# Performance work log

Measured on AMD Instinct MI355X. Metric: run time of the kernel, lower is better.

The kernel has to match this reference:

```python
import jax, jax.numpy as jnp
import numpy as np

NUM_STEPS = 32
INIT_TH = 0.125      # encoder initial threshold (args.threshold)
ENC_GROW = 2.0       # burst coding threshold growth factor
LIF_BETA = 0.9       # args.beta
LIF_TH = 1.0         # snn.Leaky default threshold
HIDDEN = 50
NUM_CLASSES = 5
DATA_STEPS = 187


def spike_fn(x):
    # Heaviside spike (forward only)
    return (x > 0).astype(x.dtype)


def setup_inputs() -> dict:
    key = jax.random.key(0)
    k1, k2, k3 = jax.random.split(key, 3)
    B = 16384
    x = jax.random.uniform(k1, (B, DATA_STEPS), dtype=jnp.float32)
    W1 = jax.random.normal(k2, (HIDDEN, DATA_STEPS), dtype=jnp.float32) * (1.0 / np.sqrt(DATA_STEPS))
    W2 = jax.random.normal(k3, (NUM_CLASSES, HIDDEN), dtype=jnp.float32) * (1.0 / np.sqrt(HIDDEN))
    return {"x": x, "W1": W1, "W2": W2}


def reference(x, W1, W2):
    B = x.shape[0]
    dt = x.dtype

    def step(carry, _):
        r, th, mem1, mem2 = carry
        # BURST encoder: spike when residual crosses adaptive threshold
        spk_in = (r >= th).astype(dt)                 # [B, D]
        r = r - spk_in * th
        th = jnp.where(spk_in > 0, th * ENC_GROW, jnp.asarray(INIT_TH, dt))
        # layer 1: linear + Leaky LIF (reset by subtraction)
        cur1 = spk_in @ W1.T                          # [B, 50]
        mem1 = LIF_BETA * mem1 + cur1
        spk1 = spike_fn(mem1 - LIF_TH)
        mem1 = mem1 - spk1 * LIF_TH
        # layer 2
        cur2 = spk1 @ W2.T                            # [B, C]
        mem2 = LIF_BETA * mem2 + cur2
        spk2 = spike_fn(mem2 - LIF_TH)
        mem2 = mem2 - spk2 * LIF_TH
        return (r, th, mem1, mem2), (spk2, spk_in.sum(1))

    carry0 = (
        x,
        jnp.full_like(x, INIT_TH),
        jnp.zeros((B, HIDDEN), dt),
        jnp.zeros((B, NUM_CLASSES), dt),
    )
    _, (spk_rec, counts) = jax.lax.scan(step, carry0, None, length=NUM_STEPS)
    # spk_rec: [T, B, C]; spike_count: [B]
    return spk_rec, counts.sum(0)
```

## Files before the change

kernel.cpp:

```cpp
#include <hip/hip_runtime.h>


constexpr int D = 187;
constexpr int H = 50;
constexpr int C = 5;
constexpr int T = 32;
constexpr int WPB = 16;
constexpr int ROWS1 = 193;
constexpr int RS = 64;

__device__ __forceinline__ int v_ffbl(unsigned int m) {
    int r;
    asm("v_ffbl_b32 %0, %1" : "=v"(r) : "v"(m));
    return r;
}

__device__ __forceinline__ void pk_add(float2& acc, float2 w) {
    asm("v_pk_add_f32 %0, %1, %0" : "+v"(acc) : "v"(w));
}

__device__ __forceinline__ void pk_fma(float2& m, float2 a, float2 c) {
    asm("v_pk_fma_f32 %0, %1, %0, %2" : "+v"(m) : "v"(a), "v"(c));
}

__device__ __forceinline__ void pk_fma_b(float2& acc, float2 s, float2 w) {
    asm("v_pk_fma_f32 %0, %2, %1, %0 op_sel:[0,0,0] op_sel_hi:[0,1,1]"
        : "+v"(acc) : "v"(w), "v"(s));
}

__device__ __forceinline__ float2 sw16(float2 v) {
    float2 r;
    r.x = __int_as_float(__builtin_amdgcn_ds_swizzle(__float_as_int(v.x), 0x401F));
    r.y = __int_as_float(__builtin_amdgcn_ds_swizzle(__float_as_int(v.y), 0x401F));
    return r;
}

__global__ __launch_bounds__(1024, 8)
void burst_snn_kernel(const float* __restrict__ x,
                      const float* __restrict__ W1,
                      const float* __restrict__ W2,
                      float* __restrict__ out, int B) {
    __shared__ float Wt1[ROWS1 * RS];
    __shared__ float Wt2[1024];

    const int tid = threadIdx.x;
    for (int idx = tid; idx < ROWS1 * RS; idx += 1024) {
        int rd = idx >> 6, j = idx & 63;
        int g = rd / 33;
        bool zrow = (rd == 33 * g);
        int d = rd - 1 - g;
        int slot = j >> 2, c = j & 3;
        int h = 13 * c + slot;
        float v = 0.f;
        if (!zrow && slot < 13 && h < H) v = W1[h * D + d];
        Wt1[idx] = v;
    }
    {
        int r = tid >> 4, c = tid & 15;
        int h = -1;
        if (r >= 1 && r <= 25) h = r - 1;
        else if (r >= 27 && r <= 51) h = r - 2;
        float v = 0.f;
        if (h >= 0 && c < C) v = W2[c * H + h];
        Wt2[tid] = v;
    }
    __syncthreads();

    const int lane = tid & 63;
    const int b = blockIdx.x * WPB + (tid >> 6);
    const bool active = b < B;
    const bool isLo = lane < 32;
    const int qOdd = (lane >> 4) & 1;
    const int ql = lane & 15;

    const char* wb = (const char*)Wt1;
    const int qbase = ql * 16 + (qOdd ? (33 << 8) : 0) + 256;
    const char* bs0 = wb + qbase;
    const char* bs1 = wb + qbase + (66 << 8);
    const char* bs2 = wb + qbase + (132 << 8);

    const float* base2 = Wt2 + ((qOdd ? 27 : 1) << 4) + ql;

    float r0 = 0.f, r1 = 0.f, r2 = 0.f;
    if (active) {
        const float* xb = x + (size_t)b * D;
        r0 = xb[lane];
        r1 = xb[64 + lane];
        if (lane < D - 128) r2 = xb[128 + lane];
    }
    float th0 = 0.125f, th1 = 0.125f, th2 = 0.125f;
    float2 m01 = make_float2(0.f, 0.f), m23 = make_float2(0.f, 0.f);
    float mem2 = 0.f;
    int cnt = 0;

    const float2 beta2 = make_float2(0.9f, 0.9f);
    const float2 neg1 = make_float2(-1.0f, -1.0f);

    float* outSpk = out;
    float* outCnt = out + (size_t)T * B * C;
    const unsigned BC = (unsigned)(B * C);
    unsigned o0 = (unsigned)(b * C + lane);

    unsigned int ga[6], gb[6];
    int tDone = T;

    for (int t = 0; t < T; t += 2) {
        {
            bool s0 = r0 >= th0, s1 = r1 >= th1, s2 = r2 >= th2;
            r0 -= s0 ? th0 : 0.f; th0 = s0 ? th0 + th0 : 0.125f;
            r1 -= s1 ? th1 : 0.f; th1 = s1 ? th1 + th1 : 0.125f;
            r2 -= s2 ? th2 : 0.f; th2 = s2 ? th2 + th2 : 0.125f;
            unsigned long long B0 = __ballot(s0), B1 = __ballot(s1), B2 = __ballot(s2);
            ga[0] = (unsigned)B0; ga[1] = (unsigned)(B0 >> 32);
            ga[2] = (unsigned)B1; ga[3] = (unsigned)(B1 >> 32);
            ga[4] = (unsigned)B2; ga[5] = (unsigned)(B2 >> 32);
        }
        {
            bool s0 = r0 >= th0, s1 = r1 >= th1, s2 = r2 >= th2;
            r0 -= s0 ? th0 : 0.f; th0 = s0 ? th0 + th0 : 0.125f;
            r1 -= s1 ? th1 : 0.f; th1 = s1 ? th1 + th1 : 0.125f;
            r2 -= s2 ? th2 : 0.f; th2 = s2 ? th2 + th2 : 0.125f;
            unsigned long long B0 = __ballot(s0), B1 = __ballot(s1), B2 = __ballot(s2);
            gb[0] = (unsigned)B0; gb[1] = (unsigned)(B0 >> 32);
            gb[2] = (unsigned)B1; gb[3] = (unsigned)(B1 >> 32);
            gb[4] = (unsigned)B2; gb[5] = (unsigned)(B2 >> 32);
        }

        int pa0 = __popc(ga[0]), pa1 = __popc(ga[1]), pa2 = __popc(ga[2]);
        int pa3 = __popc(ga[3]), pa4 = __popc(ga[4]), pa5 = __popc(ga[5]);
        int pb0 = __popc(gb[0]), pb1 = __popc(gb[1]), pb2 = __popc(gb[2]);
        int pb3 = __popc(gb[3]), pb4 = __popc(gb[4]), pb5 = __popc(gb[5]);
        cnt += pa0 + pa1 + pa2 + pa3 + pa4 + pa5
             + pb0 + pb1 + pb2 + pb3 + pb4 + pb5;
        int n = pa0 > pa1 ? pa0 : pa1;
        n = n > pa2 ? n : pa2;  n = n > pa3 ? n : pa3;
        n = n > pa4 ? n : pa4;  n = n > pa5 ? n : pa5;
        n = n > pb0 ? n : pb0;  n = n > pb1 ? n : pb1;
        n = n > pb2 ? n : pb2;  n = n > pb3 ? n : pb3;
        n = n > pb4 ? n : pb4;  n = n > pb5 ? n : pb5;

        unsigned e0 = isLo ? ga[0] : gb[0], d0 = isLo ? ga[1] : gb[1];
        unsigned e1 = isLo ? ga[2] : gb[2], d1 = isLo ? ga[3] : gb[3];
        unsigned e2 = isLo ? ga[4] : gb[4], d2 = isLo ? ga[5] : gb[5];
        unsigned vm0 = qOdd ? d0 : e0;
        unsigned vm1 = qOdd ? d1 : e1;
        unsigned vm2 = qOdd ? d2 : e2;

        float2 a0l = {0.f, 0.f}, a0h = {0.f, 0.f};
        float2 a1l = {0.f, 0.f}, a1h = {0.f, 0.f};
        float2 a2l = {0.f, 0.f}, a2h = {0.f, 0.f};
        if (n >= 21) {
            float2 sv0 = {0.f, 0.f}, sv1 = {0.f, 0.f}, sv2 = {0.f, 0.f};
            #pragma unroll
            for (int f = 0; f < 32; ++f) {
                sv0.x = (float)((vm0 >> f) & 1u);
                sv1.x = (float)((vm1 >> f) & 1u);
                sv2.x = (float)((vm2 >> f) & 1u);
                const char* p0 = bs0 + (f << 8);
                const char* p1 = bs1 + (f << 8);
                const char* p2 = bs2 + (f << 8);
                float2 w0l = *(const float2*)p0, w0h = *(const float2*)(p0 + 8);
                float2 w1l = *(const float2*)p1, w1h = *(const float2*)(p1 + 8);
                float2 w2l = *(const float2*)p2, w2h = *(const float2*)(p2 + 8);
                pk_fma_b(a0l, sv0, w0l); pk_fma_b(a0h, sv0, w0h);
                pk_fma_b(a1l, sv1, w1l); pk_fma_b(a1h, sv1, w1h);
                pk_fma_b(a2l, sv2, w2l); pk_fma_b(a2h, sv2, w2h);
            }
        } else {
            for (; n > 0; --n) {
                int f0 = v_ffbl(vm0); vm0 &= vm0 - 1;
                int f1 = v_ffbl(vm1); vm1 &= vm1 - 1;
                int f2 = v_ffbl(vm2); vm2 &= vm2 - 1;
                const char* p0 = bs0 + (f0 << 8);
                const char* p1 = bs1 + (f1 << 8);
                const char* p2 = bs2 + (f2 << 8);
                float2 w0l = *(const float2*)p0, w0h = *(const float2*)(p0 + 8);
                float2 w1l = *(const float2*)p1, w1h = *(const float2*)(p1 + 8);
                float2 w2l = *(const float2*)p2, w2h = *(const float2*)(p2 + 8);
                pk_add(a0l, w0l); pk_add(a0h, w0h);
                pk_add(a1l, w1l); pk_add(a1h, w1h);
                pk_add(a2l, w2l); pk_add(a2h, w2h);
            }
        }

        float2 s0l = sw16(a0l), s0h = sw16(a0h);
        float2 s1l = sw16(a1l), s1h = sw16(a1h);
        float2 s2l = sw16(a2l), s2h = sw16(a2h);
        float2 cml = a0l, cmh = a0h;
        pk_add(cml, s0l); pk_add(cmh, s0h);
        pk_add(cml, a1l); pk_add(cmh, a1h);
        pk_add(cml, s1l); pk_add(cmh, s1h);
        pk_add(cml, a2l); pk_add(cmh, a2h);
        pk_add(cml, s2l); pk_add(cmh, s2h);
        float2 cu01 = make_float2(__shfl_down(cml.x, 32), __shfl_down(cml.y, 32));
        float2 cu23 = make_float2(__shfl_down(cmh.x, 32), __shfl_down(cmh.y, 32));

        pk_fma(m01, beta2, cml);
        pk_fma(m23, beta2, cmh);
        float2 d01 = m01, d23 = m23;
        pk_add(d01, neg1); pk_add(d23, neg1);
        bool t0 = d01.x > 0.f, t1 = d01.y > 0.f;
        bool t2 = d23.x > 0.f, t3 = d23.y > 0.f;
        unsigned long long Pa = __ballot(t0), Pb = __ballot(t1);
        unsigned long long Pc = __ballot(t2), Pd = __ballot(t3);
        m01.x = t0 ? d01.x : m01.x;  m01.y = t1 ? d01.y : m01.y;
        m23.x = t2 ? d23.x : m23.x;  m23.y = t3 ? d23.y : m23.y;
        unsigned c0t = (unsigned)Pa & 0x1FFFu;
        unsigned c1t = (unsigned)Pb & 0x1FFFu;
        unsigned c2t = (unsigned)Pc & 0x1FFFu;
        unsigned c3t = (unsigned)Pd & 0x1FFFu;
        pk_fma(m01, beta2, cu01);
        pk_fma(m23, beta2, cu23);
        float2 e01 = m01, e23 = m23;
        pk_add(e01, neg1); pk_add(e23, neg1);
        bool u0 = e01.x > 0.f, u1 = e01.y > 0.f;
        bool u2 = e23.x > 0.f, u3 = e23.y > 0.f;
        unsigned long long Qa = __ballot(u0), Qb = __ballot(u1);
        unsigned long long Qc = __ballot(u2), Qd = __ballot(u3);
        m01.x = u0 ? e01.x : m01.x;  m01.y = u1 ? e01.y : m01.y;
        m23.x = u2 ? e23.x : m23.x;  m23.y = u3 ? e23.y : m23.y;
        unsigned c0u = (unsigned)Qa & 0x1FFFu;
        unsigned c1u = (unsigned)Qb & 0x1FFFu;
        unsigned c2u = (unsigned)Qc & 0x1FFFu;
        unsigned c3u = (unsigned)Qd & 0x1FFFu;

        unsigned lo_t = c0t | ((c1t & 0xFFFu) << 13);
        unsigned hi_t = (c1t >> 12) | (c2t << 1) | ((c3t & 0x7FFu) << 14);
        unsigned lo_u = c0u | ((c1u & 0xFFFu) << 13);
        unsigned hi_u = (c1u >> 12) | (c2u << 1) | ((c3u & 0x7FFu) << 14);

        int p0c = __popc(lo_t), p1c = __popc(hi_t);
        int p2c = __popc(lo_u), p3c = __popc(hi_u);
        int n2 = p0c > p1c ? p0c : p1c;
        n2 = n2 > p2c ? n2 : p2c;
        n2 = n2 > p3c ? n2 : p3c;
        float cq = 0.f;
        if (n2) {
            unsigned vmq = isLo ? (qOdd ? hi_t : lo_t) : (qOdd ? hi_u : lo_u);
            for (; n2 > 0; --n2) {
                int f = v_ffbl(vmq); vmq &= vmq - 1;
                cq += *(base2 + f * 16);
            }
        }
        float tmp = cq + __shfl_down(cq, 16);
        float cur2 = tmp;
        float c2t1 = __shfl_down(tmp, 32);

        mem2 = 0.9f * mem2 + cur2;
        bool sp2 = (mem2 - 1.0f > 0.f);
        mem2 -= sp2 ? 1.0f : 0.f;
        if (active && lane < C) outSpk[o0] = sp2 ? 1.0f : 0.0f;
        mem2 = 0.9f * mem2 + c2t1;
        bool sp2b = (mem2 - 1.0f > 0.f);
        mem2 -= sp2b ? 1.0f : 0.f;
        if (active && lane < C) outSpk[o0 + BC] = sp2b ? 1.0f : 0.0f;
        o0 += 2u * BC;

        unsigned encAny = ga[0] | ga[1] | ga[2] | ga[3] | ga[4] | ga[5]
                        | gb[0] | gb[1] | gb[2] | gb[3] | gb[4] | gb[5];
        unsigned l1Any = lo_t | hi_t | lo_u | hi_u;
        if ((encAny | l1Any) == 0u) {
            float rm = fmaxf(fmaxf(r0, r1), r2);
            unsigned long long am = __ballot(rm >= 0.125f);
            float mm = fmaxf(fmaxf(m01.x, m01.y), fmaxf(m23.x, m23.y));
            unsigned long long m1 = __ballot(mm > 1.0f) & 0x1FFFull;
            unsigned long long m2 = __ballot(mem2 > 1.0f) & 0x1Full;
            if ((am | m1 | m2) == 0ull) { tDone = t + 2; break; }
        }
    }

    if (active && lane < C) {
        for (int tt = tDone; tt < T; ++tt) {
            outSpk[o0] = 0.0f;
            o0 += BC;
        }
    }
    if (active && lane == 0) outCnt[b] = (float)cnt;
}

extern "C" void kernel_launch(void* const* d_in, const int* in_sizes, int n_in,
                              void* d_out, int out_size, void* d_ws, size_t ws_size,
                              hipStream_t stream) {
    const float* x  = (const float*)d_in[0];
    const float* W1 = (const float*)d_in[1];
    const float* W2 = (const float*)d_in[2];
    float* out = (float*)d_out;
    const int B = in_sizes[0] / D;
    const int blocks = (B + WPB - 1) / WPB;
    burst_snn_kernel<<<blocks, 1024, 0, stream>>>(x, W1, W2, out, B);
}
```

Before: 121.3 us.

## Process two batch rows per wavefront, each half-wave owning one row

Each 64-lane wave now handles two samples instead of one: the lower and upper 32 lanes each hold one row's 187 inputs across six registers. Layer-1 work pairs the two samples within one time step instead of pairing two time steps of one sample, and the output write, spike count and early-exit masks are split per half-wave. This halves the number of blocks and is meant to spread the serial time-step and sparse-gather overhead over twice as many samples. In exchange each lane carries more registers, and the data-dependent gather loop count becomes the max over two samples, so it may run longer.

Measured after the change: 122.7 us. No clear change (+1.1%).

```diff
diff --git a/kernel.cpp b/kernel.cpp
--- a/kernel.cpp
+++ b/kernel.cpp
@@ -6,6 +6,7 @@
 constexpr int C = 5;
 constexpr int T = 32;
 constexpr int WPB = 16;
+constexpr int EPB = WPB * 2;
 constexpr int ROWS1 = 193;
 constexpr int RS = 64;
 
@@ -67,9 +68,10 @@
     __syncthreads();
 
     const int lane = tid & 63;
-    const int b = blockIdx.x * WPB + (tid >> 6);
+    const int laneH = lane & 31;
+    const bool isLo = lane < 32;
+    const int b = blockIdx.x * EPB + ((tid >> 6) << 1) + (isLo ? 0 : 1);
     const bool active = b < B;
-    const bool isLo = lane < 32;
     const int qOdd = (lane >> 4) & 1;
     const int ql = lane & 15;
 
@@ -81,17 +83,21 @@
 
     const float* base2 = Wt2 + ((qOdd ? 27 : 1) << 4) + ql;
 
-    float r0 = 0.f, r1 = 0.f, r2 = 0.f;
+    float r0 = 0.f, r1 = 0.f, r2 = 0.f, r3 = 0.f, r4 = 0.f, r5 = 0.f;
     if (active) {
         const float* xb = x + (size_t)b * D;
-        r0 = xb[lane];
-        r1 = xb[64 + lane];
-        if (lane < D - 128) r2 = xb[128 + lane];
+        r0 = xb[laneH];
+        r1 = xb[32 + laneH];
+        r2 = xb[64 + laneH];
+        r3 = xb[96 + laneH];
+        r4 = xb[128 + laneH];
+        if (laneH < D - 160) r5 = xb[160 + laneH];
     }
     float th0 = 0.125f, th1 = 0.125f, th2 = 0.125f;
+    float th3 = 0.125f, th4 = 0.125f, th5 = 0.125f;
     float2 m01 = make_float2(0.f, 0.f), m23 = make_float2(0.f, 0.f);
     float mem2 = 0.f;
-    int cnt = 0;
+    int cntA = 0, cntB = 0;
 
     const float2 beta2 = make_float2(0.9f, 0.9f);
     const float2 neg1 = make_float2(-1.0f, -1.0f);
@@ -99,53 +105,12 @@
     float* outSpk = out;
     float* outCnt = out + (size_t)T * B * C;
     const unsigned BC = (unsigned)(B * C);
-    unsigned o0 = (unsigned)(b * C + lane);
-
-    unsigned int ga[6], gb[6];
+    unsigned o0 = (unsigned)(b * C + laneH);
+
     int tDone = T;
 
-    for (int t = 0; t < T; t += 2) {
-        {
-            bool s0 = r0 >= th0, s1 = r1 >= th1, s2 = r2 >= th2;
-            r0 -= s0 ? th0 : 0.f; th0 = s0 ? th0 + th0 : 0.125f;
-            r1 -= s1 ? th1 : 0.f; th1 = s1 ? th1 + th1 : 0.125f;
-            r2 -= s2 ? th2 : 0.f; th2 = s2 ? th2 + th2 : 0.125f;
-            unsigned long long B0 = __ballot(s0), B1 = __ballot(s1), B2 = __ballot(s2);
-            ga[0] = (unsigned)B0; ga[1] = (unsigned)(B0 >> 32);
-            ga[2] = (unsigned)B1; ga[3] = (unsigned)(B1 >> 32);
-            ga[4] = (unsigned)B2; ga[5] = (unsigned)(B2 >> 32);
-        }
-        {
-            bool s0 = r0 >= th0, s1 = r1 >= th1, s2 = r2 >= th2;
-            r0 -= s0 ? th0 : 0.f; th0 = s0 ? th0 + th0 : 0.125f;
-            r1 -= s1 ? th1 : 0.f; th1 = s1 ? th1 + th1 : 0.125f;
-            r2 -= s2 ? th2 : 0.f; th2 = s2 ? th2 + th2 : 0.125f;
-            unsigned long long B0 = __ballot(s0), B1 = __ballot(s1), B2 = __ballot(s2);
-            gb[0] = (unsigned)B0; gb[1] = (unsigned)(B0 >> 32);
-            gb[2] = (unsigned)B1; gb[3] = (unsigned)(B1 >> 32);
-            gb[4] = (unsigned)B2; gb[5] = (unsigned)(B2 >> 32);
-        }
-
-        int pa0 = __popc(ga[0]), pa1 = __popc(ga[1]), pa2 = __popc(ga[2]);
-        int pa3 = __popc(ga[3]), pa4 = __popc(ga[4]), pa5 = __popc(ga[5]);
-        int pb0 = __popc(gb[0]), pb1 = __popc(gb[1]), pb2 = __popc(gb[2]);
-        int pb3 = __popc(gb[3]), pb4 = __popc(gb[4]), pb5 = __popc(gb[5]);
-        cnt += pa0 + pa1 + pa2 + pa3 + pa4 + pa5
-             + pb0 + pb1 + pb2 + pb3 + pb4 + pb5;
-        int n = pa0 > pa1 ? pa0 : pa1;
-        n = n > pa2 ? n : pa2;  n = n > pa3 ? n : pa3;
-        n = n > pa4 ? n : pa4;  n = n > pa5 ? n : pa5;
-        n = n > pb0 ? n : pb0;  n = n > pb1 ? n : pb1;
-        n = n > pb2 ? n : pb2;  n = n > pb3 ? n : pb3;
-        n = n > pb4 ? n : pb4;  n = n > pb5 ? n : pb5;
-
-        unsigned e0 = isLo ? ga[0] : gb[0], d0 = isLo ? ga[1] : gb[1];
-        unsigned e1 = isLo ? ga[2] : gb[2], d1 = isLo ? ga[3] : gb[3];
-        unsigned e2 = isLo ? ga[4] : gb[4], d2 = isLo ? ga[5] : gb[5];
-        unsigned vm0 = qOdd ? d0 : e0;
-        unsigned vm1 = qOdd ? d1 : e1;
-        unsigned vm2 = qOdd ? d2 : e2;
-
+    auto gather = [&](unsigned vm0, unsigned vm1, unsigned vm2, int n,
+                      float2& cml, float2& cmh) {
         float2 a0l = {0.f, 0.f}, a0h = {0.f, 0.f};
         float2 a1l = {0.f, 0.f}, a1h = {0.f, 0.f};
         float2 a2l = {0.f, 0.f}, a2h = {0.f, 0.f};
@@ -182,19 +147,19 @@
                 pk_add(a2l, w2l); pk_add(a2h, w2h);
             }
         }
-
         float2 s0l = sw16(a0l), s0h = sw16(a0h);
         float2 s1l = sw16(a1l), s1h = sw16(a1h);
         float2 s2l = sw16(a2l), s2h = sw16(a2h);
-        float2 cml = a0l, cmh = a0h;
+        cml = a0l; cmh = a0h;
         pk_add(cml, s0l); pk_add(cmh, s0h);
         pk_add(cml, a1l); pk_add(cmh, a1h);
         pk_add(cml, s1l); pk_add(cmh, s1h);
         pk_add(cml, a2l); pk_add(cmh, a2h);
         pk_add(cml, s2l); pk_add(cmh, s2h);
-        float2 cu01 = make_float2(__shfl_down(cml.x, 32), __shfl_down(cml.y, 32));
-        float2 cu23 = make_float2(__shfl_down(cmh.x, 32), __shfl_down(cmh.y, 32));
-
+    };
+
+    auto lif1 = [&](float2 cml, float2 cmh, unsigned& loA, unsigned& hiA,
+                    unsigned& loB, unsigned& hiB) {
         pk_fma(m01, beta2, cml);
         pk_fma(m23, beta2, cmh);
         float2 d01 = m01, d23 = m23;
@@ -205,77 +170,151 @@
         unsigned long long Pc = __ballot(t2), Pd = __ballot(t3);
         m01.x = t0 ? d01.x : m01.x;  m01.y = t1 ? d01.y : m01.y;
         m23.x = t2 ? d23.x : m23.x;  m23.y = t3 ? d23.y : m23.y;
-        unsigned c0t = (unsigned)Pa & 0x1FFFu;
-        unsigned c1t = (unsigned)Pb & 0x1FFFu;
-        unsigned c2t = (unsigned)Pc & 0x1FFFu;
-        unsigned c3t = (unsigned)Pd & 0x1FFFu;
-        pk_fma(m01, beta2, cu01);
-        pk_fma(m23, beta2, cu23);
-        float2 e01 = m01, e23 = m23;
-        pk_add(e01, neg1); pk_add(e23, neg1);
-        bool u0 = e01.x > 0.f, u1 = e01.y > 0.f;
-        bool u2 = e23.x > 0.f, u3 = e23.y > 0.f;
-        unsigned long long Qa = __ballot(u0), Qb = __ballot(u1);
-        unsigned long long Qc = __ballot(u2), Qd = __ballot(u3);
-        m01.x = u0 ? e01.x : m01.x;  m01.y = u1 ? e01.y : m01.y;
-        m23.x = u2 ? e23.x : m23.x;  m23.y = u3 ? e23.y : m23.y;
-        unsigned c0u = (unsigned)Qa & 0x1FFFu;
-        unsigned c1u = (unsigned)Qb & 0x1FFFu;
-        unsigned c2u = (unsigned)Qc & 0x1FFFu;
-        unsigned c3u = (unsigned)Qd & 0x1FFFu;
-
-        unsigned lo_t = c0t | ((c1t & 0xFFFu) << 13);
-        unsigned hi_t = (c1t >> 12) | (c2t << 1) | ((c3t & 0x7FFu) << 14);
-        unsigned lo_u = c0u | ((c1u & 0xFFFu) << 13);
-        unsigned hi_u = (c1u >> 12) | (c2u << 1) | ((c3u & 0x7FFu) << 14);
-
-        int p0c = __popc(lo_t), p1c = __popc(hi_t);
-        int p2c = __popc(lo_u), p3c = __popc(hi_u);
-        int n2 = p0c > p1c ? p0c : p1c;
-        n2 = n2 > p2c ? n2 : p2c;
-        n2 = n2 > p3c ? n2 : p3c;
+        unsigned cA0 = (unsigned)Pa & 0x1FFFu, cB0 = (unsigned)(Pa >> 32) & 0x1FFFu;
+        unsigned cA1 = (unsigned)Pb & 0x1FFFu, cB1 = (unsigned)(Pb >> 32) & 0x1FFFu;
+        unsigned cA2 = (unsigned)Pc & 0x1FFFu, cB2 = (unsigned)(Pc >> 32) & 0x1FFFu;
+        unsigned cA3 = (unsigned)Pd & 0x1FFFu, cB3 = (unsigned)(Pd >> 32) & 0x1FFFu;
+        loA = cA0 | ((cA1 & 0xFFFu) << 13);
+        hiA = (cA1 >> 12) | (cA2 << 1) | ((cA3 & 0x7FFu) << 14);
+        loB = cB0 | ((cB1 & 0xFFFu) << 13);
+        hiB = (cB1 >> 12) | (cB2 << 1) | ((cB3 & 0x7FFu) << 14);
+    };
+
+    auto l2step = [&](unsigned loA, unsigned hiA, unsigned loB, unsigned hiB) {
+        int p0 = __popc(loA), p1 = __popc(hiA);
+        int p2 = __popc(loB), p3 = __popc(hiB);
+        int n2 = p0 > p1 ? p0 : p1;
+        n2 = n2 > p2 ? n2 : p2;
+        n2 = n2 > p3 ? n2 : p3;
         float cq = 0.f;
         if (n2) {
-            unsigned vmq = isLo ? (qOdd ? hi_t : lo_t) : (qOdd ? hi_u : lo_u);
+            unsigned vmq = isLo ? (qOdd ? hiA : loA) : (qOdd ? hiB : loB);
             for (; n2 > 0; --n2) {
                 int f = v_ffbl(vmq); vmq &= vmq - 1;
                 cq += *(base2 + f * 16);
             }
         }
-        float tmp = cq + __shfl_down(cq, 16);
-        float cur2 = tmp;
-        float c2t1 = __shfl_down(tmp, 32);
-
+        float cur2 = cq + __shfl_down(cq, 16);
         mem2 = 0.9f * mem2 + cur2;
         bool sp2 = (mem2 - 1.0f > 0.f);
         mem2 -= sp2 ? 1.0f : 0.f;
-        if (active && lane < C) outSpk[o0] = sp2 ? 1.0f : 0.0f;
-        mem2 = 0.9f * mem2 + c2t1;
-        bool sp2b = (mem2 - 1.0f > 0.f);
-        mem2 -= sp2b ? 1.0f : 0.f;
-        if (active && lane < C) outSpk[o0 + BC] = sp2b ? 1.0f : 0.0f;
-        o0 += 2u * BC;
-
-        unsigned encAny = ga[0] | ga[1] | ga[2] | ga[3] | ga[4] | ga[5]
-                        | gb[0] | gb[1] | gb[2] | gb[3] | gb[4] | gb[5];
-        unsigned l1Any = lo_t | hi_t | lo_u | hi_u;
-        if ((encAny | l1Any) == 0u) {
-            float rm = fmaxf(fmaxf(r0, r1), r2);
+        if (active && laneH < C) outSpk[o0] = sp2 ? 1.0f : 0.0f;
+        o0 += BC;
+    };
+
+    for (int t = 0; t < T; t += 2) {
+        unsigned long long E0, E1, E2, E3, E4, E5;
+        {
+            bool s0 = r0 >= th0, s1 = r1 >= th1, s2 = r2 >= th2;
+            bool s3 = r3 >= th3, s4 = r4 >= th4, s5 = r5 >= th5;
+            r0 -= s0 ? th0 : 0.f; th0 = s0 ? th0 + th0 : 0.125f;
+            r1 -= s1 ? th1 : 0.f; th1 = s1 ? th1 + th1 : 0.125f;
+            r2 -= s2 ? th2 : 0.f; th2 = s2 ? th2 + th2 : 0.125f;
+            r3 -= s3 ? th3 : 0.f; th3 = s3 ? th3 + th3 : 0.125f;
+            r4 -= s4 ? th4 : 0.f; th4 = s4 ? th4 + th4 : 0.125f;
+            r5 -= s5 ? th5 : 0.f; th5 = s5 ? th5 + th5 : 0.125f;
+            E0 = __ballot(s0); E1 = __ballot(s1); E2 = __ballot(s2);
+            E3 = __ballot(s3); E4 = __ballot(s4); E5 = __ballot(s5);
+        }
+        unsigned long long F0, F1, F2, F3, F4, F5;
+        {
+            bool s0 = r0 >= th0, s1 = r1 >= th1, s2 = r2 >= th2;
+            bool s3 = r3 >= th3, s4 = r4 >= th4, s5 = r5 >= th5;
+            r0 -= s0 ? th0 : 0.f; th0 = s0 ? th0 + th0 : 0.125f;
+            r1 -= s1 ? th1 : 0.f; th1 = s1 ? th1 + th1 : 0.125f;
+            r2 -= s2 ? th2 : 0.f; th2 = s2 ? th2 + th2 : 0.125f;
+            r3 -= s3 ? th3 : 0.f; th3 = s3 ? th3 + th3 : 0.125f;
+            r4 -= s4 ? th4 : 0.f; th4 = s4 ? th4 + th4 : 0.125f;
+            r5 -= s5 ? th5 : 0.f; th5 = s5 ? th5 + th5 : 0.125f;
+            F0 = __ballot(s0); F1 = __ballot(s1); F2 = __ballot(s2);
+            F3 = __ballot(s3); F4 = __ballot(s4); F5 = __ballot(s5);
+        }
+
+        unsigned At0 = (unsigned)E0, Bt0 = (unsigned)(E0 >> 32);
+        unsigned At1 = (unsigned)E1, Bt1 = (unsigned)(E1 >> 32);
+        unsigned At2 = (unsigned)E2, Bt2 = (unsigned)(E2 >> 32);
+        unsigned At3 = (unsigned)E3, Bt3 = (unsigned)(E3 >> 32);
+        unsigned At4 = (unsigned)E4, Bt4 = (unsigned)(E4 >> 32);
+        unsigned At5 = (unsigned)E5, Bt5 = (unsigned)(E5 >> 32);
+        unsigned Au0 = (unsigned)F0, Bu0 = (unsigned)(F0 >> 32);
+        unsigned Au1 = (unsigned)F1, Bu1 = (unsigned)(F1 >> 32);
+        unsigned Au2 = (unsigned)F2, Bu2 = (unsigned)(F2 >> 32);
+        unsigned Au3 = (unsigned)F3, Bu3 = (unsigned)(F3 >> 32);
+        unsigned Au4 = (unsigned)F4, Bu4 = (unsigned)(F4 >> 32);
+        unsigned Au5 = (unsigned)F5, Bu5 = (unsigned)(F5 >> 32);
+
+        int qa0 = __popc(At0), qa1 = __popc(At1), qa2 = __popc(At2);
+        int qa3 = __popc(At3), qa4 = __popc(At4), qa5 = __popc(At5);
+        int qb0 = __popc(Bt0), qb1 = __popc(Bt1), qb2 = __popc(Bt2);
+        int qb3 = __popc(Bt3), qb4 = __popc(Bt4), qb5 = __popc(Bt5);
+        int ra0 = __popc(Au0), ra1 = __popc(Au1), ra2 = __popc(Au2);
+        int ra3 = __popc(Au3), ra4 = __popc(Au4), ra5 = __popc(Au5);
+        int rb0 = __popc(Bu0), rb1 = __popc(Bu1), rb2 = __popc(Bu2);
+        int rb3 = __popc(Bu3), rb4 = __popc(Bu4), rb5 = __popc(Bu5);
+        cntA += qa0 + qa1 + qa2 + qa3 + qa4 + qa5
+              + ra0 + ra1 + ra2 + ra3 + ra4 + ra5;
+        cntB += qb0 + qb1 + qb2 + qb3 + qb4 + qb5
+              + rb0 + rb1 + rb2 + rb3 + rb4 + rb5;
+        int nt = qa0 > qa1 ? qa0 : qa1;
+        nt = nt > qa2 ? nt : qa2;  nt = nt > qa3 ? nt : qa3;
+        nt = nt > qa4 ? nt : qa4;  nt = nt > qa5 ? nt : qa5;
+        nt = nt > qb0 ? nt : qb0;  nt = nt > qb1 ? nt : qb1;
+        nt = nt > qb2 ? nt : qb2;  nt = nt > qb3 ? nt : qb3;
+        nt = nt > qb4 ? nt : qb4;  nt = nt > qb5 ? nt : qb5;
+        int nu = ra0 > ra1 ? ra0 : ra1;
+        nu = nu > ra2 ? nu : ra2;  nu = nu > ra3 ? nu : ra3;
+        nu = nu > ra4 ? nu : ra4;  nu = nu > ra5 ? nu : ra5;
+        nu = nu > rb0 ? nu : rb0;  nu = nu > rb1 ? nu : rb1;
+        nu = nu > rb2 ? nu : rb2;  nu = nu > rb3 ? nu : rb3;
+        nu = nu > rb4 ? nu : rb4;  nu = nu > rb5 ? nu : rb5;
+
+        unsigned g0 = isLo ? At0 : Bt0, g1 = isLo ? At1 : Bt1;
+        unsigned g2 = isLo ? At2 : Bt2, g3 = isLo ? At3 : Bt3;
+        unsigned g4 = isLo ? At4 : Bt4, g5 = isLo ? At5 : Bt5;
+        unsigned vmt0 = qOdd ? g1 : g0;
+        unsigned vmt1 = qOdd ? g3 : g2;
+        unsigned vmt2 = qOdd ? g5 : g4;
+
+        float2 cml, cmh;
+        gather(vmt0, vmt1, vmt2, nt, cml, cmh);
+        unsigned loAt, hiAt, loBt, hiBt;
+        lif1(cml, cmh, loAt, hiAt, loBt, hiBt);
+
+        unsigned h0 = isLo ? Au0 : Bu0, h1 = isLo ? Au1 : Bu1;
+        unsigned h2 = isLo ? Au2 : Bu2, h3 = isLo ? Au3 : Bu3;
+        unsigned h4 = isLo ? Au4 : Bu4, h5 = isLo ? Au5 : Bu5;
+        unsigned vmu0 = qOdd ? h1 : h0;
+        unsigned vmu1 = qOdd ? h3 : h2;
+        unsigned vmu2 = qOdd ? h5 : h4;
+
+        gather(vmu0, vmu1, vmu2, nu, cml, cmh);
+        unsigned loAu, hiAu, loBu, hiBu;
+        lif1(cml, cmh, loAu, hiAu, loBu, hiBu);
+
+        l2step(loAt, hiAt, loBt, hiBt);
+        l2step(loAu, hiAu, loBu, hiBu);
+
+        unsigned long long encAny = E0 | E1 | E2 | E3 | E4 | E5
+                                  | F0 | F1 | F2 | F3 | F4 | F5;
+        unsigned l1Any = loAt | hiAt | loBt | hiBt
+                       | loAu | hiAu | loBu | hiBu;
+        if ((encAny | (unsigned long long)l1Any) == 0ull) {
+            float rm = fmaxf(fmaxf(fmaxf(r0, r1), fmaxf(r2, r3)), fmaxf(r4, r5));
             unsigned long long am = __ballot(rm >= 0.125f);
             float mm = fmaxf(fmaxf(m01.x, m01.y), fmaxf(m23.x, m23.y));
-            unsigned long long m1 = __ballot(mm > 1.0f) & 0x1FFFull;
-            unsigned long long m2 = __ballot(mem2 > 1.0f) & 0x1Full;
+            unsigned long long m1 = __ballot(mm > 1.0f) & 0x00001FFF00001FFFull;
+            unsigned long long m2 = __ballot(mem2 > 1.0f) & 0x0000001F0000001Full;
             if ((am | m1 | m2) == 0ull) { tDone = t + 2; break; }
         }
     }
 
-    if (active && lane < C) {
+    if (active && laneH < C) {
         for (int tt = tDone; tt < T; ++tt) {
             outSpk[o0] = 0.0f;
             o0 += BC;
         }
     }
-    if (active && lane == 0) outCnt[b] = (float)cnt;
+    if (active && laneH == 0) outCnt[b] = (float)(isLo ? cntA : cntB);
 }
 
 extern "C" void kernel_launch(void* const* d_in, const int* in_sizes, int n_in,
@@ -286,6 +325,6 @@
     const float* W2 = (const float*)d_in[2];
     float* out = (float*)d_out;
     const int B = in_sizes[0] / D;
-    const int blocks = (B + WPB - 1) / WPB;
+    const int blocks = (B + EPB - 1) / EPB;
     burst_snn_kernel<<<blocks, 1024, 0, stream>>>(x, W1, W2, out, B);
 }
```

## Use persistent blocks with atomic work-stealing over batch rows

Applied to the files above, without the earlier changes.

Switches from one wavefront per row with a full grid to a persistent grid capped at 512 blocks. Each wavefront claims its next batch row through a global atomic counter, which is reset with a memset in the workspace before launch. The aim is to balance work across rows whose early-exit times differ and to build the LDS weight tables once per block instead of once per 16 rows. It adds an atomic per row, an extra memset launch, and a loop-carried register state that could lower occupancy.

New measurement: 267.5 us. +120.5%, slower.

```diff
diff --git a/kernel.cpp b/kernel.cpp
--- a/kernel.cpp
+++ b/kernel.cpp
@@ -39,7 +39,8 @@
 void burst_snn_kernel(const float* __restrict__ x,
                       const float* __restrict__ W1,
                       const float* __restrict__ W2,
-                      float* __restrict__ out, int B) {
+                      float* __restrict__ out,
+                      int* __restrict__ counter, int B) {
     __shared__ float Wt1[ROWS1 * RS];
     __shared__ float Wt2[1024];
 
@@ -67,8 +68,6 @@
     __syncthreads();
 
     const int lane = tid & 63;
-    const int b = blockIdx.x * WPB + (tid >> 6);
-    const bool active = b < B;
     const bool isLo = lane < 32;
     const int qOdd = (lane >> 4) & 1;
     const int ql = lane & 15;
@@ -81,201 +80,207 @@
 
     const float* base2 = Wt2 + ((qOdd ? 27 : 1) << 4) + ql;
 
-    float r0 = 0.f, r1 = 0.f, r2 = 0.f;
-    if (active) {
-        const float* xb = x + (size_t)b * D;
-        r0 = xb[lane];
-        r1 = xb[64 + lane];
-        if (lane < D - 128) r2 = xb[128 + lane];
-    }
-    float th0 = 0.125f, th1 = 0.125f, th2 = 0.125f;
-    float2 m01 = make_float2(0.f, 0.f), m23 = make_float2(0.f, 0.f);
-    float mem2 = 0.f;
-    int cnt = 0;
-
     const float2 beta2 = make_float2(0.9f, 0.9f);
     const float2 neg1 = make_float2(-1.0f, -1.0f);
 
     float* outSpk = out;
     float* outCnt = out + (size_t)T * B * C;
     const unsigned BC = (unsigned)(B * C);
-    unsigned o0 = (unsigned)(b * C + lane);
-
-    unsigned int ga[6], gb[6];
-    int tDone = T;
-
-    for (int t = 0; t < T; t += 2) {
-        {
-            bool s0 = r0 >= th0, s1 = r1 >= th1, s2 = r2 >= th2;
-            r0 -= s0 ? th0 : 0.f; th0 = s0 ? th0 + th0 : 0.125f;
-            r1 -= s1 ? th1 : 0.f; th1 = s1 ? th1 + th1 : 0.125f;
-            r2 -= s2 ? th2 : 0.f; th2 = s2 ? th2 + th2 : 0.125f;
-            unsigned long long B0 = __ballot(s0), B1 = __ballot(s1), B2 = __ballot(s2);
-            ga[0] = (unsigned)B0; ga[1] = (unsigned)(B0 >> 32);
-            ga[2] = (unsigned)B1; ga[3] = (unsigned)(B1 >> 32);
-            ga[4] = (unsigned)B2; ga[5] = (unsigned)(B2 >> 32);
+    const int Bstart = gridDim.x * WPB;
+
+    int b = blockIdx.x * WPB + (tid >> 6);
+
+    while (b < B) {
+        const float* xb = x + (size_t)b * D;
+        float r0 = xb[lane];
+        float r1 = xb[64 + lane];
+        float r2 = (lane < D - 128) ? xb[128 + lane] : 0.f;
+        float th0 = 0.125f, th1 = 0.125f, th2 = 0.125f;
+        float2 m01 = make_float2(0.f, 0.f), m23 = make_float2(0.f, 0.f);
+        float mem2 = 0.f;
+        int cnt = 0;
+        unsigned o0 = (unsigned)(b * C + lane);
+        unsigned int ga[6], gb[6];
+        int tDone = T;
+
+        for (int t = 0; t < T; t += 2) {
+            {
+                bool s0 = r0 >= th0, s1 = r1 >= th1, s2 = r2 >= th2;
+                r0 -= s0 ? th0 : 0.f; th0 = s0 ? th0 + th0 : 0.125f;
+                r1 -= s1 ? th1 : 0.f; th1 = s1 ? th1 + th1 : 0.125f;
+                r2 -= s2 ? th2 : 0.f; th2 = s2 ? th2 + th2 : 0.125f;
+                unsigned long long B0 = __ballot(s0), B1 = __ballot(s1), B2 = __ballot(s2);
+                ga[0] = (unsigned)B0; ga[1] = (unsigned)(B0 >> 32);
+                ga[2] = (unsigned)B1; ga[3] = (unsigned)(B1 >> 32);
+                ga[4] = (unsigned)B2; ga[5] = (unsigned)(B2 >> 32);
+            }
+            {
+                bool s0 = r0 >= th0, s1 = r1 >= th1, s2 = r2 >= th2;
+                r0 -= s0 ? th0 : 0.f; th0 = s0 ? th0 + th0 : 0.125f;
+                r1 -= s1 ? th1 : 0.f; th1 = s1 ? th1 + th1 : 0.125f;
+                r2 -= s2 ? th2 : 0.f; th2 = s2 ? th2 + th2 : 0.125f;
+                unsigned long long B0 = __ballot(s0), B1 = __ballot(s1), B2 = __ballot(s2);
+                gb[0] = (unsigned)B0; gb[1] = (unsigned)(B0 >> 32);
+                gb[2] = (unsigned)B1; gb[3] = (unsigned)(B1 >> 32);
+                gb[4] = (unsigned)B2; gb[5] = (unsigned)(B2 >> 32);
+            }
+
+            int pa0 = __popc(ga[0]), pa1 = __popc(ga[1]), pa2 = __popc(ga[2]);
+            int pa3 = __popc(ga[3]), pa4 = __popc(ga[4]), pa5 = __popc(ga[5]);
+            int pb0 = __popc(gb[0]), pb1 = __popc(gb[1]), pb2 = __popc(gb[2]);
+            int pb3 = __popc(gb[3]), pb4 = __popc(gb[4]), pb5 = __popc(gb[5]);
+            cnt += pa0 + pa1 + pa2 + pa3 + pa4 + pa5
+                 + pb0 + pb1 + pb2 + pb3 + pb4 + pb5;
+            int n = pa0 > pa1 ? pa0 : pa1;
+            n = n > pa2 ? n : pa2;  n = n > pa3 ? n : pa3;
+            n = n > pa4 ? n : pa4;  n = n > pa5 ? n : pa5;
+            n = n > pb0 ? n : pb0;  n = n > pb1 ? n : pb1;
+            n = n > pb2 ? n : pb2;  n = n > pb3 ? n : pb3;
+            n = n > pb4 ? n : pb4;  n = n > pb5 ? n : pb5;
+
+            unsigned e0 = isLo ? ga[0] : gb[0], d0 = isLo ? ga[1] : gb[1];
+            unsigned e1 = isLo ? ga[2] : gb[2], d1 = isLo ? ga[3] : gb[3];
+            unsigned e2 = isLo ? ga[4] : gb[4], d2 = isLo ? ga[5] : gb[5];
+            unsigned vm0 = qOdd ? d0 : e0;
+            unsigned vm1 = qOdd ? d1 : e1;
+            unsigned vm2 = qOdd ? d2 : e2;
+
+            float2 a0l = {0.f, 0.f}, a0h = {0.f, 0.f};
+            float2 a1l = {0.f, 0.f}, a1h = {0.f, 0.f};
+            float2 a2l = {0.f, 0.f}, a2h = {0.f, 0.f};
+            if (n >= 21) {
+                float2 sv0 = {0.f, 0.f}, sv1 = {0.f, 0.f}, sv2 = {0.f, 0.f};
+                #pragma unroll
+                for (int f = 0; f < 32; ++f) {
+                    sv0.x = (float)((vm0 >> f) & 1u);
+                    sv1.x = (float)((vm1 >> f) & 1u);
+                    sv2.x = (float)((vm2 >> f) & 1u);
+                    const char* p0 = bs0 + (f << 8);
+                    const char* p1 = bs1 + (f << 8);
+                    const char* p2 = bs2 + (f << 8);
+                    float2 w0l = *(const float2*)p0, w0h = *(const float2*)(p0 + 8);
+                    float2 w1l = *(const float2*)p1, w1h = *(const float2*)(p1 + 8);
+                    float2 w2l = *(const float2*)p2, w2h = *(const float2*)(p2 + 8);
+                    pk_fma_b(a0l, sv0, w0l); pk_fma_b(a0h, sv0, w0h);
+                    pk_fma_b(a1l, sv1, w1l); pk_fma_b(a1h, sv1, w1h);
+                    pk_fma_b(a2l, sv2, w2l); pk_fma_b(a2h, sv2, w2h);
+                }
+            } else {
+                for (; n > 0; --n) {
+                    int f0 = v_ffbl(vm0); vm0 &= vm0 - 1;
+                    int f1 = v_ffbl(vm1); vm1 &= vm1 - 1;
+                    int f2 = v_ffbl(vm2); vm2 &= vm2 - 1;
+                    const char* p0 = bs0 + (f0 << 8);
+                    const char* p1 = bs1 + (f1 << 8);
+                    const char* p2 = bs2 + (f2 << 8);
+                    float2 w0l = *(const float2*)p0, w0h = *(const float2*)(p0 + 8);
+                    float2 w1l = *(const float2*)p1, w1h = *(const float2*)(p1 + 8);
+                    float2 w2l = *(const float2*)p2, w2h = *(const float2*)(p2 + 8);
+                    pk_add(a0l, w0l); pk_add(a0h, w0h);
+                    pk_add(a1l, w1l); pk_add(a1h, w1h);
+                    pk_add(a2l, w2l); pk_add(a2h, w2h);
+                }
+            }
+
+            float2 s0l = sw16(a0l), s0h = sw16(a0h);
+            float2 s1l = sw16(a1l), s1h = sw16(a1h);
+            float2 s2l = sw16(a2l), s2h = sw16(a2h);
+            float2 cml = a0l, cmh = a0h;
+            pk_add(cml, s0l); pk_add(cmh, s0h);
+            pk_add(cml, a1l); pk_add(cmh, a1h);
+            pk_add(cml, s1l); pk_add(cmh, s1h);
+            pk_add(cml, a2l); pk_add(cmh, a2h);
+            pk_add(cml, s2l); pk_add(cmh, s2h);
+            float2 cu01 = make_float2(__shfl_down(cml.x, 32), __shfl_down(cml.y, 32));
+            float2 cu23 = make_float2(__shfl_down(cmh.x, 32), __shfl_down(cmh.y, 32));
+
+            pk_fma(m01, beta2, cml);
+            pk_fma(m23, beta2, cmh);
+            float2 d01 = m01, d23 = m23;
+            pk_add(d01, neg1); pk_add(d23, neg1);
+            bool t0 = d01.x > 0.f, t1 = d01.y > 0.f;
+            bool t2 = d23.x > 0.f, t3 = d23.y > 0.f;
+            unsigned long long Pa = __ballot(t0), Pb = __ballot(t1);
+            unsigned long long Pc = __ballot(t2), Pd = __ballot(t3);
+            m01.x = t0 ? d01.x : m01.x;  m01.y = t1 ? d01.y : m01.y;
+            m23.x = t2 ? d23.x : m23.x;  m23.y = t3 ? d23.y : m23.y;
+            unsigned c0t = (unsigned)Pa & 0x1FFFu;
+            unsigned c1t = (unsigned)Pb & 0x1FFFu;
+            unsigned c2t = (unsigned)Pc & 0x1FFFu;
+            unsigned c3t = (unsigned)Pd & 0x1FFFu;
+            pk_fma(m01, beta2, cu01);
+            pk_fma(m23, beta2, cu23);
+            float2 e01 = m01, e23 = m23;
+            pk_add(e01, neg1); pk_add(e23, neg1);
+            bool u0 = e01.x > 0.f, u1 = e01.y > 0.f;
+            bool u2 = e23.x > 0.f, u3 = e23.y > 0.f;
+            unsigned long long Qa = __ballot(u0), Qb = __ballot(u1);
+            unsigned long long Qc = __ballot(u2), Qd = __ballot(u3);
+            m01.x = u0 ? e01.x : m01.x;  m01.y = u1 ? e01.y : m01.y;
+            m23.x = u2 ? e23.x : m23.x;  m23.y = u3 ? e23.y : m23.y;
+            unsigned c0u = (unsigned)Qa & 0x1FFFu;
+            unsigned c1u = (unsigned)Qb & 0x1FFFu;
+            unsigned c2u = (unsigned)Qc & 0x1FFFu;
+            unsigned c3u = (unsigned)Qd & 0x1FFFu;
+
+            unsigned lo_t = c0t | ((c1t & 0xFFFu) << 13);
+            unsigned hi_t = (c1t >> 12) | (c2t << 1) | ((c3t & 0x7FFu) << 14);
+            unsigned lo_u = c0u | ((c1u & 0xFFFu) << 13);
+            unsigned hi_u = (c1u >> 12) | (c2u << 1) | ((c3u & 0x7FFu) << 14);
+
+            int p0c = __popc(lo_t), p1c = __popc(hi_t);
+            int p2c = __popc(lo_u), p3c = __popc(hi_u);
+            int n2 = p0c > p1c ? p0c : p1c;
+            n2 = n2 > p2c ? n2 : p2c;
+            n2 = n2 > p3c ? n2 : p3c;
+            float cq = 0.f;
+            if (n2) {
+                unsigned vmq = isLo ? (qOdd ? hi_t : lo_t) : (qOdd ? hi_u : lo_u);
+                for (; n2 > 0; --n2) {
+                    int f = v_ffbl(vmq); vmq &= vmq - 1;
+                    cq += *(base2 + f * 16);
+                }
+            }
+            float tmp = cq + __shfl_down(cq, 16);
+            float cur2 = tmp;
+            float c2t1 = __shfl_down(tmp, 32);
+
+            mem2 = 0.9f * mem2 + cur2;
+            bool sp2 = (mem2 - 1.0f > 0.f);
+            mem2 -= sp2 ? 1.0f : 0.f;
+            if (lane < C) outSpk[o0] = sp2 ? 1.0f : 0.0f;
+            mem2 = 0.9f * mem2 + c2t1;
+            bool sp2b = (mem2 - 1.0f > 0.f);
+            mem2 -= sp2b ? 1.0f : 0.f;
+            if (lane < C) outSpk[o0 + BC] = sp2b ? 1.0f : 0.0f;
+            o0 += 2u * BC;
+
+            unsigned encAny = ga[0] | ga[1] | ga[2] | ga[3] | ga[4] | ga[5]
+                            | gb[0] | gb[1] | gb[2] | gb[3] | gb[4] | gb[5];
+            unsigned l1Any = lo_t | hi_t | lo_u | hi_u;
+            if ((encAny | l1Any) == 0u) {
+                float rm = fmaxf(fmaxf(r0, r1), r2);
+                unsigned long long am = __ballot(rm >= 0.125f);
+                float mm = fmaxf(fmaxf(m01.x, m01.y), fmaxf(m23.x, m23.y));
+                unsigned long long m1 = __ballot(mm > 1.0f) & 0x1FFFull;
+                unsigned long long m2 = __ballot(mem2 > 1.0f) & 0x1Full;
+                if ((am | m1 | m2) == 0ull) { tDone = t + 2; break; }
+            }
         }
-        {
-            bool s0 = r0 >= th0, s1 = r1 >= th1, s2 = r2 >= th2;
-            r0 -= s0 ? th0 : 0.f; th0 = s0 ? th0 + th0 : 0.125f;
-            r1 -= s1 ? th1 : 0.f; th1 = s1 ? th1 + th1 : 0.125f;
-            r2 -= s2 ? th2 : 0.f; th2 = s2 ? th2 + th2 : 0.125f;
-            unsigned long long B0 = __ballot(s0), B1 = __ballot(s1), B2 = __ballot(s2);
-            gb[0] = (unsigned)B0; gb[1] = (unsigned)(B0 >> 32);
-            gb[2] = (unsigned)B1; gb[3] = (unsigned)(B1 >> 32);
-            gb[4] = (unsigned)B2; gb[5] = (unsigned)(B2 >> 32);
+
+        if (lane < C) {
+            for (int tt = tDone; tt < T; ++tt) {
+                outSpk[o0] = 0.0f;
+                o0 += BC;
+            }
         }
-
-        int pa0 = __popc(ga[0]), pa1 = __popc(ga[1]), pa2 = __popc(ga[2]);
-        int pa3 = __popc(ga[3]), pa4 = __popc(ga[4]), pa5 = __popc(ga[5]);
-        int pb0 = __popc(gb[0]), pb1 = __popc(gb[1]), pb2 = __popc(gb[2]);
-        int pb3 = __popc(gb[3]), pb4 = __popc(gb[4]), pb5 = __popc(gb[5]);
-        cnt += pa0 + pa1 + pa2 + pa3 + pa4 + pa5
-             + pb0 + pb1 + pb2 + pb3 + pb4 + pb5;
-        int n = pa0 > pa1 ? pa0 : pa1;
-        n = n > pa2 ? n : pa2;  n = n > pa3 ? n : pa3;
-        n = n > pa4 ? n : pa4;  n = n > pa5 ? n : pa5;
-        n = n > pb0 ? n : pb0;  n = n > pb1 ? n : pb1;
-        n = n > pb2 ? n : pb2;  n = n > pb3 ? n : pb3;
-        n = n > pb4 ? n : pb4;  n = n > pb5 ? n : pb5;
-
-        unsigned e0 = isLo ? ga[0] : gb[0], d0 = isLo ? ga[1] : gb[1];
-        unsigned e1 = isLo ? ga[2] : gb[2], d1 = isLo ? ga[3] : gb[3];
-        unsigned e2 = isLo ? ga[4] : gb[4], d2 = isLo ? ga[5] : gb[5];
-        unsigned vm0 = qOdd ? d0 : e0;
-        unsigned vm1 = qOdd ? d1 : e1;
-        unsigned vm2 = qOdd ? d2 : e2;
-
-        float2 a0l = {0.f, 0.f}, a0h = {0.f, 0.f};
-        float2 a1l = {0.f, 0.f}, a1h = {0.f, 0.f};
-        float2 a2l = {0.f, 0.f}, a2h = {0.f, 0.f};
-        if (n >= 21) {
-            float2 sv0 = {0.f, 0.f}, sv1 = {0.f, 0.f}, sv2 = {0.f, 0.f};
-            #pragma unroll
-            for (int f = 0; f < 32; ++f) {
-                sv0.x = (float)((vm0 >> f) & 1u);
-                sv1.x = (float)((vm1 >> f) & 1u);
-                sv2.x = (float)((vm2 >> f) & 1u);
-                const char* p0 = bs0 + (f << 8);
-                const char* p1 = bs1 + (f << 8);
-                const char* p2 = bs2 + (f << 8);
-                float2 w0l = *(const float2*)p0, w0h = *(const float2*)(p0 + 8);
-                float2 w1l = *(const float2*)p1, w1h = *(const float2*)(p1 + 8);
-                float2 w2l = *(const float2*)p2, w2h = *(const float2*)(p2 + 8);
-                pk_fma_b(a0l, sv0, w0l); pk_fma_b(a0h, sv0, w0h);
-                pk_fma_b(a1l, sv1, w1l); pk_fma_b(a1h, sv1, w1h);
-                pk_fma_b(a2l, sv2, w2l); pk_fma_b(a2h, sv2, w2h);
-            }
-        } else {
-            for (; n > 0; --n) {
-                int f0 = v_ffbl(vm0); vm0 &= vm0 - 1;
-                int f1 = v_ffbl(vm1); vm1 &= vm1 - 1;
-                int f2 = v_ffbl(vm2); vm2 &= vm2 - 1;
-                const char* p0 = bs0 + (f0 << 8);
-                const char* p1 = bs1 + (f1 << 8);
-                const char* p2 = bs2 + (f2 << 8);
-                float2 w0l = *(const float2*)p0, w0h = *(const float2*)(p0 + 8);
-                float2 w1l = *(const float2*)p1, w1h = *(const float2*)(p1 + 8);
-                float2 w2l = *(const float2*)p2, w2h = *(const float2*)(p2 + 8);
-                pk_add(a0l, w0l); pk_add(a0h, w0h);
-                pk_add(a1l, w1l); pk_add(a1h, w1h);
-                pk_add(a2l, w2l); pk_add(a2h, w2h);
-            }
-        }
-
-        float2 s0l = sw16(a0l), s0h = sw16(a0h);
-        float2 s1l = sw16(a1l), s1h = sw16(a1h);
-        float2 s2l = sw16(a2l), s2h = sw16(a2h);
-        float2 cml = a0l, cmh = a0h;
-        pk_add(cml, s0l); pk_add(cmh, s0h);
-        pk_add(cml, a1l); pk_add(cmh, a1h);
-        pk_add(cml, s1l); pk_add(cmh, s1h);
-        pk_add(cml, a2l); pk_add(cmh, a2h);
-        pk_add(cml, s2l); pk_add(cmh, s2h);
-        float2 cu01 = make_float2(__shfl_down(cml.x, 32), __shfl_down(cml.y, 32));
-        float2 cu23 = make_float2(__shfl_down(cmh.x, 32), __shfl_down(cmh.y, 32));
-
-        pk_fma(m01, beta2, cml);
-        pk_fma(m23, beta2, cmh);
-        float2 d01 = m01, d23 = m23;
-        pk_add(d01, neg1); pk_add(d23, neg1);
-        bool t0 = d01.x > 0.f, t1 = d01.y > 0.f;
-        bool t2 = d23.x > 0.f, t3 = d23.y > 0.f;
-        unsigned long long Pa = __ballot(t0), Pb = __ballot(t1);
-        unsigned long long Pc = __ballot(t2), Pd = __ballot(t3);
-        m01.x = t0 ? d01.x : m01.x;  m01.y = t1 ? d01.y : m01.y;
-        m23.x = t2 ? d23.x : m23.x;  m23.y = t3 ? d23.y : m23.y;
-        unsigned c0t = (unsigned)Pa & 0x1FFFu;
-        unsigned c1t = (unsigned)Pb & 0x1FFFu;
-        unsigned c2t = (unsigned)Pc & 0x1FFFu;
-        unsigned c3t = (unsigned)Pd & 0x1FFFu;
-        pk_fma(m01, beta2, cu01);
-        pk_fma(m23, beta2, cu23);
-        float2 e01 = m01, e23 = m23;
-        pk_add(e01, neg1); pk_add(e23, neg1);
-        bool u0 = e01.x > 0.f, u1 = e01.y > 0.f;
-        bool u2 = e23.x > 0.f, u3 = e23.y > 0.f;
-        unsigned long long Qa = __ballot(u0), Qb = __ballot(u1);
-        unsigned long long Qc = __ballot(u2), Qd = __ballot(u3);
-        m01.x = u0 ? e01.x : m01.x;  m01.y = u1 ? e01.y : m01.y;
-        m23.x = u2 ? e23.x : m23.x;  m23.y = u3 ? e23.y : m23.y;
-        unsigned c0u = (unsigned)Qa & 0x1FFFu;
-        unsigned c1u = (unsigned)Qb & 0x1FFFu;
-        unsigned c2u = (unsigned)Qc & 0x1FFFu;
-        unsigned c3u = (unsigned)Qd & 0x1FFFu;
-
-        unsigned lo_t = c0t | ((c1t & 0xFFFu) << 13);
-        unsigned hi_t = (c1t >> 12) | (c2t << 1) | ((c3t & 0x7FFu) << 14);
-        unsigned lo_u = c0u | ((c1u & 0xFFFu) << 13);
-        unsigned hi_u = (c1u >> 12) | (c2u << 1) | ((c3u & 0x7FFu) << 14);
-
-        int p0c = __popc(lo_t), p1c = __popc(hi_t);
-        int p2c = __popc(lo_u), p3c = __popc(hi_u);
-        int n2 = p0c > p1c ? p0c : p1c;
-        n2 = n2 > p2c ? n2 : p2c;
-        n2 = n2 > p3c ? n2 : p3c;
-        float cq = 0.f;
-        if (n2) {
-            unsigned vmq = isLo ? (qOdd ? hi_t : lo_t) : (qOdd ? hi_u : lo_u);
-            for (; n2 > 0; --n2) {
-                int f = v_ffbl(vmq); vmq &= vmq - 1;
-                cq += *(base2 + f * 16);
-            }
-        }
-        float tmp = cq + __shfl_down(cq, 16);
-        float cur2 = tmp;
-        float c2t1 = __shfl_down(tmp, 32);
-
-        mem2 = 0.9f * mem2 + cur2;
-        bool sp2 = (mem2 - 1.0f > 0.f);
-        mem2 -= sp2 ? 1.0f : 0.f;
-        if (active && lane < C) outSpk[o0] = sp2 ? 1.0f : 0.0f;
-        mem2 = 0.9f * mem2 + c2t1;
-        bool sp2b = (mem2 - 1.0f > 0.f);
-        mem2 -= sp2b ? 1.0f : 0.f;
-        if (active && lane < C) outSpk[o0 + BC] = sp2b ? 1.0f : 0.0f;
-        o0 += 2u * BC;
-
-        unsigned encAny = ga[0] | ga[1] | ga[2] | ga[3] | ga[4] | ga[5]
-                        | gb[0] | gb[1] | gb[2] | gb[3] | gb[4] | gb[5];
-        unsigned l1Any = lo_t | hi_t | lo_u | hi_u;
-        if ((encAny | l1Any) == 0u) {
-            float rm = fmaxf(fmaxf(r0, r1), r2);
-            unsigned long long am = __ballot(rm >= 0.125f);
-            float mm = fmaxf(fmaxf(m01.x, m01.y), fmaxf(m23.x, m23.y));
-            unsigned long long m1 = __ballot(mm > 1.0f) & 0x1FFFull;
-            unsigned long long m2 = __ballot(mem2 > 1.0f) & 0x1Full;
-            if ((am | m1 | m2) == 0ull) { tDone = t + 2; break; }
-        }
+        if (lane == 0) outCnt[b] = (float)cnt;
+
+        int nxt;
+        if (lane == 0) nxt = atomicAdd(counter, 1);
+        nxt = __shfl(nxt, 0);
+        b = Bstart + nxt;
     }
-
-    if (active && lane < C) {
-        for (int tt = tDone; tt < T; ++tt) {
-            outSpk[o0] = 0.0f;
-            o0 += BC;
-        }
-    }
-    if (active && lane == 0) outCnt[b] = (float)cnt;
 }
 
 extern "C" void kernel_launch(void* const* d_in, const int* in_sizes, int n_in,
@@ -286,6 +291,9 @@
     const float* W2 = (const float*)d_in[2];
     float* out = (float*)d_out;
     const int B = in_sizes[0] / D;
-    const int blocks = (B + WPB - 1) / WPB;
-    burst_snn_kernel<<<blocks, 1024, 0, stream>>>(x, W1, W2, out, B);
-}
+    int blocks = (B + WPB - 1) / WPB;
+    if (blocks > 512) blocks = 512;
+    hipMemsetAsync(d_ws, 0, sizeof(int), stream);
+    burst_snn_kernel<<<blocks, 1024, 0, stream>>>(x, W1, W2, out,
+                                                  (int*)d_ws, B);
+}
```
